# Performance work log

Measured on AMD Instinct MI355X. Metric: run time of the kernel, lower is better.

The kernel has to match this reference:

```python
import jax, jax.numpy as jnp
import numpy as np


def fwht(x):
    """Fast Walsh-Hadamard transform over the last dim (power of 2), normalized by 1/sqrt(n)."""
    n = x.shape[-1]
    orig_shape = x.shape
    x = x.reshape(-1, n)
    h = 1
    while h < n:
        x = x.reshape(-1, n // (2 * h), 2, h)
        a = x[:, :, 0, :]
        b = x[:, :, 1, :]
        x = jnp.stack([a + b, a - b], axis=2)
        h *= 2
    x = x.reshape(orig_shape)
    return x * (1.0 / jnp.sqrt(jnp.asarray(n, dtype=x.dtype)))


def act_quant(x, bits):
    """Per-token absmax symmetric quantization with straight-through estimator."""
    qb = 2.0 ** (bits - 1) - 1.0  # 127 for 8 bits
    scale = qb / jnp.clip(jnp.max(jnp.abs(x), axis=-1, keepdims=True), 1e-5, None)
    q = jnp.clip(jnp.round(x * scale), -qb, qb) / scale
    return x + jax.lax.stop_gradient(q - x)


def weight_quant(w):
    """BitNet b1.58 ternary weight quantization (per-tensor mean-abs scale) with STE."""
    scale = jnp.clip(jnp.mean(jnp.abs(w)), 1e-5, None)
    q = jnp.clip(jnp.round(w / scale), -1.0, 1.0) * scale
    return w + jax.lax.stop_gradient(q - w)


def hbitlinear(x, w, bits):
    # Hadamard rotate activations, quantize acts + ternary weights, then GEMM.
    xh = fwht(x)
    xq = act_quant(xh, bits)
    wq = weight_quant(w)
    return jnp.einsum('bsh,oh->bso', xq, wq)


def setup_inputs() -> dict:
    key = jax.random.key(0)
    k1, k2, k3 = jax.random.split(key, 3)
    B, S, H = 4, 2048, 2048
    I = 4096  # intermediate = hidden * mlp_ratio(2.0)
    hidden_states = jax.random.normal(k1, (B, S, H), dtype=jnp.float32)
    w_up = jax.random.normal(k2, (I, H), dtype=jnp.float32) * 0.02
    w_down = jax.random.normal(k3, (H, I), dtype=jnp.float32) * 0.02
    return {"hidden_states": hidden_states, "w_up": w_up, "w_down": w_down}


def reference(hidden_states, w_up, w_down):
    ACT_BITS = 8
    h = hbitlinear(hidden_states, w_up, ACT_BITS)   # (B, S, I)
    h = jnp.square(jax.nn.relu(h))                  # ReLU^2
    # dropout with p=0.0 (eval/identity)
    out = hbitlinear(h, w_down, ACT_BITS)           # (B, S, H)
    return out
```

## Files before the change

kernel.cpp:

```cpp
#include <hip/hip_runtime.h>
#include <hip/hip_bf16.h>

typedef int i32x4 __attribute__((ext_vector_type(4)));

#define BM 128
#define BN 128
#define BK 64

#define GLL16(g, l) __builtin_amdgcn_global_load_lds( \
    (const __attribute__((address_space(1))) void*)(g), \
    (__attribute__((address_space(3))) void*)(l), 16, 0, 0)

__global__ __launch_bounds__(256) void abs_sum_kernel(const float* __restrict__ w, int n4,
                                                      double* __restrict__ out)
{
    double acc = 0.0;
    const float4* w4 = (const float4*)w;
    for (int i = blockIdx.x * blockDim.x + threadIdx.x; i < n4; i += gridDim.x * blockDim.x) {
        float4 v = w4[i];
        acc += (double)fabsf(v.x) + (double)fabsf(v.y) + (double)fabsf(v.z) + (double)fabsf(v.w);
    }
    for (int o = 32; o > 0; o >>= 1) acc += __shfl_down(acc, o, 64);
    __shared__ double part[4];
    int lane = threadIdx.x & 63, wv = threadIdx.x >> 6;
    if (lane == 0) part[wv] = acc;
    __syncthreads();
    if (threadIdx.x == 0) atomicAdd(out, part[0] + part[1] + part[2] + part[3]);
}

__global__ __launch_bounds__(256) void wquant_kernel(const float* __restrict__ w, int n4,
                                                     const double* __restrict__ sum, double inv_count,
                                                     char* __restrict__ out)
{
    float s = (float)(sum[0] * inv_count);
    s = fmaxf(s, 1e-5f);
    const float4* w4 = (const float4*)w;
    char4* o4 = (char4*)out;
    for (int i = blockIdx.x * blockDim.x + threadIdx.x; i < n4; i += gridDim.x * blockDim.x) {
        float4 v = w4[i];
        char4 c;
        c.x = (char)fminf(fmaxf(rintf(v.x / s), -1.0f), 1.0f);
        c.y = (char)fminf(fmaxf(rintf(v.y / s), -1.0f), 1.0f);
        c.z = (char)fminf(fmaxf(rintf(v.z / s), -1.0f), 1.0f);
        c.w = (char)fminf(fmaxf(rintf(v.w / s), -1.0f), 1.0f);
        o4[i] = c;
    }
}

template<int NS>
__device__ __forceinline__ void hreg(float* v)
{
    #pragma unroll
    for (int h = 1; h < (1 << NS); h <<= 1)
        #pragma unroll
        for (int i = 0; i < 16; i++)
            if ((i & h) == 0) { float a = v[i], b = v[i + h]; v[i] = a + b; v[i + h] = a - b; }
}

template<int N, int TOKS>
__global__ __launch_bounds__(256) void fwht_quant_kernel(
    const float* __restrict__ in, long in_stride,
    char* __restrict__ outq, long out_stride,
    float* __restrict__ scales)
{
    constexpr int L = 256 / TOKS;
    static_assert(N == 16 * L, "N must be 16*threads-per-token");
    __shared__ float sx[TOKS * N];
    __shared__ float red[4];

    const int tid = threadIdx.x;
    const int tk  = tid / L;
    const int lt  = tid % L;
    const long tok = (long)blockIdx.x * TOKS + tk;
    const float* row = in + tok * in_stride;
    float* s = sx + tk * N;

    float v[16];
    {
        const float4* r4 = (const float4*)(row + (size_t)lt * 16);
        float4 a[4];
        #pragma unroll
        for (int i = 0; i < 4; i++) a[i] = r4[i];
        #pragma unroll
        for (int i = 0; i < 4; i++) {
            v[4*i] = a[i].x; v[4*i+1] = a[i].y; v[4*i+2] = a[i].z; v[4*i+3] = a[i].w;
        }
    }
    hreg<4>(v);
    #pragma unroll
    for (int i = 0; i < 4; i++)
        *(float4*)(s + lt * 16 + 4 * i) = make_float4(v[4*i], v[4*i+1], v[4*i+2], v[4*i+3]);
    __syncthreads();

    const int o = lt & 15, ss = lt >> 4;
    #pragma unroll
    for (int j = 0; j < 16; j++) v[j] = s[o + 256 * ss + 16 * j];
    hreg<(L == 256) ? 4 : 3>(v);
    #pragma unroll
    for (int j = 0; j < 16; j++) s[o + 256 * ss + 16 * j] = v[j];
    __syncthreads();

    #pragma unroll
    for (int j = 0; j < 16; j++) v[j] = s[o + 16 * ss + L * j];
    hreg<4>(v);

    const float rn = 1.0f / sqrtf((float)N);
    float m = 0.0f;
    #pragma unroll
    for (int j = 0; j < 16; j++) { v[j] *= rn; m = fmaxf(m, fabsf(v[j])); }
    for (int off = 32; off > 0; off >>= 1) m = fmaxf(m, __shfl_down(m, off, 64));
    if ((tid & 63) == 0) red[tid >> 6] = m;
    __syncthreads();
    float mm;
    if (TOKS == 1) mm = fmaxf(fmaxf(red[0], red[1]), fmaxf(red[2], red[3]));
    else           mm = fmaxf(red[2 * tk], red[2 * tk + 1]);
    mm = fmaxf(mm, 1e-5f);
    const float sc = 127.0f / mm;
    if (lt == 0) scales[tok] = sc;
    __syncthreads();

    char* ct = (char*)sx + tk * N;
    #pragma unroll
    for (int j = 0; j < 16; j++) {
        float q = fminf(fmaxf(rintf(v[j] * sc), -127.0f), 127.0f);
        ct[o + 16 * ss + L * j] = (char)q;
    }
    __syncthreads();
    int4* dst = (int4*)(outq + tok * out_stride);
    dst[lt] = ((const int4*)ct)[lt];
}

__global__ __launch_bounds__(256) void gemm_bt_kernel(
    const char* __restrict__ A, int lda,
    const char* __restrict__ B, int ldb,
    float* __restrict__ C, int ldc,
    int K, int lognx,
    const float* __restrict__ sx,
    const double* __restrict__ wsum, double inv_count,
    int do_relu2)
{
    __shared__ __align__(16) char As[2][BM * BK];
    __shared__ __align__(16) char Bs[2][BN * BK];

    const int bid = blockIdx.x;
    const int xcd = bid & 7;
    const int n = bid >> 3;
    const int nper = gridDim.x >> 3;
    const int bx = n & ((1 << lognx) - 1);
    const int by = xcd * (nper >> lognx) + (n >> lognx);
    const int row0 = by * BM;
    const int col0 = bx * BN;

    const int tid = threadIdx.x;
    const int lane = tid & 63;
    const int wave = tid >> 6;
    const int wm = (wave >> 1) * 64;
    const int wn = (wave & 1) * 64;

    i32x4 acc[4][4] = {};

    const int srow = wave * 16 + (lane >> 2);
    const int scol = (lane & 3) * 16;
    const char* Ag = A + (size_t)(row0 + srow) * lda + scol;
    const char* Bg = B + (size_t)(col0 + srow) * ldb + scol;
    const size_t ldA64 = (size_t)64 * lda, ldB64 = (size_t)64 * ldb;
    const int wb0 = (wave * 16) * BK;
    const int wb1 = (wave * 16 + 64) * BK;

    const int fr = lane & 15;
    const int fk = (lane >> 4) * 16;

    for (int k0 = 0; k0 < K; k0 += 2 * BK) {
        __syncthreads();
        GLL16(Ag + k0,              &As[0][wb0]);
        GLL16(Ag + k0 + ldA64,      &As[0][wb1]);
        GLL16(Bg + k0,              &Bs[0][wb0]);
        GLL16(Bg + k0 + ldB64,      &Bs[0][wb1]);
        GLL16(Ag + k0 + BK,         &As[1][wb0]);
        GLL16(Ag + k0 + BK + ldA64, &As[1][wb1]);
        GLL16(Bg + k0 + BK,         &Bs[1][wb0]);
        GLL16(Bg + k0 + BK + ldB64, &Bs[1][wb1]);
        __syncthreads();

        #pragma unroll
        for (int p = 0; p < 2; p++) {
            i32x4 af[4], bfr[4];
            #pragma unroll
            for (int i = 0; i < 4; i++) {
                af[i]  = *(const i32x4*)(&As[p][(wm + i * 16 + fr) * BK + fk]);
                bfr[i] = *(const i32x4*)(&Bs[p][(wn + i * 16 + fr) * BK + fk]);
            }
            #pragma unroll
            for (int i = 0; i < 4; i++)
                #pragma unroll
                for (int j = 0; j < 4; j++)
                    acc[i][j] = __builtin_amdgcn_mfma_i32_16x16x64_i8(af[i], bfr[j], acc[i][j], 0, 0, 0);
        }
    }

    float sw = (float)(wsum[0] * inv_count);
    sw = fmaxf(sw, 1e-5f);
    const int qd = lane >> 4;
    #pragma unroll
    for (int i = 0; i < 4; i++) {
        #pragma unroll
        for (int r = 0; r < 4; r++) {
            int rowm = row0 + wm + i * 16 + qd * 4 + r;
            float esc = sw / sx[rowm];
            float* crow = C + (size_t)rowm * ldc + col0 + wn;
            #pragma unroll
            for (int j = 0; j < 4; j++) {
                float v = (float)acc[i][j][r] * esc;
                if (do_relu2) { v = fmaxf(v, 0.0f); v = v * v; }
                crow[j * 16 + fr] = v;
            }
        }
    }
}

extern "C" void kernel_launch(void* const* d_in, const int* in_sizes, int n_in,
                              void* d_out, int out_size, void* d_ws, size_t ws_size,
                              hipStream_t stream)
{
    const float* X   = (const float*)d_in[0];
    const float* Wup = (const float*)d_in[1];
    const float* Wdn = (const float*)d_in[2];
    float* out = (float*)d_out;

    const int Mtok = 8192, H = 2048, I = 4096;
    const int NW = H * I;

    char* ws = (char*)d_ws;
    double* sums = (double*)ws;
    float* sx1 = (float*)(ws + 1024);
    float* sx2 = (float*)(ws + 1024 + 32768);
    char* wqup = ws + (1 << 20);
    char* wqdn = wqup + (size_t)NW;
    char* xq1  = wqdn + (size_t)NW;
    float* hbuf = (float*)(xq1 + (size_t)Mtok * H);

    hipMemsetAsync(sums, 0, 16, stream);
    abs_sum_kernel<<<512, 256, 0, stream>>>(Wup, NW / 4, &sums[0]);
    abs_sum_kernel<<<512, 256, 0, stream>>>(Wdn, NW / 4, &sums[1]);
    const double invc = 1.0 / (double)NW;
    wquant_kernel<<<1024, 256, 0, stream>>>(Wup, NW / 4, &sums[0], invc, wqup);
    wquant_kernel<<<1024, 256, 0, stream>>>(Wdn, NW / 4, &sums[1], invc, wqdn);

    fwht_quant_kernel<2048, 2><<<Mtok / 2, 256, 0, stream>>>(X, H, xq1, H, sx1);
    gemm_bt_kernel<<<(I / BN) * (Mtok / BM), 256, 0, stream>>>(
        xq1, H, wqup, H, hbuf, I, H, 5, sx1, &sums[0], invc, 1);
    fwht_quant_kernel<4096, 1><<<Mtok, 256, 0, stream>>>(hbuf, I, (char*)hbuf, 4 * I, sx2);
    gemm_bt_kernel<<<(H / BN) * (Mtok / BM), 256, 0, stream>>>(
        (const char*)hbuf, 4 * I, wqdn, I, out, H, I, 4, sx2, &sums[1], invc, 0);
}
```

Before: 406.2 us.

## Enlarge int8 GEMM tiles to 256x256 with 4-stage LDS pipeline and swizzle

Reworks the int8 MFMA GEMM to 256x256 block tiles over 8 waves. Global-to-LDS loads now run through a 4-buffer ring that keeps three stages in flight, synchronised with explicit vmcnt waits and barriers. An XOR swizzle on LDS addresses is meant to avoid bank conflicts, and setprio raises priority around the MFMA bursts. The goal is more data reuse per block and better overlap of loads with compute. The cost is 128KB of LDS per block and fewer blocks in the grid, so occupancy and the tail effect become risks.

After: 405.8 us. Within noise of the previous version (-0.1%).

```diff
diff --git a/kernel.cpp b/kernel.cpp
--- a/kernel.cpp
+++ b/kernel.cpp
@@ -2,14 +2,12 @@
 #include <hip/hip_bf16.h>
 
 typedef int i32x4 __attribute__((ext_vector_type(4)));
-
-#define BM 128
-#define BN 128
-#define BK 64
 
 #define GLL16(g, l) __builtin_amdgcn_global_load_lds( \
     (const __attribute__((address_space(1))) void*)(g), \
     (__attribute__((address_space(3))) void*)(l), 16, 0, 0)
+
+#define CFENCE() asm volatile("" ::: "memory")
 
 __global__ __launch_bounds__(256) void abs_sum_kernel(const float* __restrict__ w, int n4,
                                                       double* __restrict__ out)
@@ -130,7 +128,11 @@
     dst[lt] = ((const int4*)ct)[lt];
 }
 
-__global__ __launch_bounds__(256) void gemm_bt_kernel(
+#define BM2 256
+#define BN2 256
+#define BK2 64
+
+__global__ __launch_bounds__(512, 2) void gemm_bt_kernel(
     const char* __restrict__ A, int lda,
     const char* __restrict__ B, int ldb,
     float* __restrict__ C, int ldc,
@@ -139,8 +141,8 @@
     const double* __restrict__ wsum, double inv_count,
     int do_relu2)
 {
-    __shared__ __align__(16) char As[2][BM * BK];
-    __shared__ __align__(16) char Bs[2][BN * BK];
+    __shared__ __align__(16) char As[4][BM2 * BK2];
+    __shared__ __align__(16) char Bs[4][BN2 * BK2];
 
     const int bid = blockIdx.x;
     const int xcd = bid & 7;
@@ -148,68 +150,95 @@
     const int nper = gridDim.x >> 3;
     const int bx = n & ((1 << lognx) - 1);
     const int by = xcd * (nper >> lognx) + (n >> lognx);
-    const int row0 = by * BM;
-    const int col0 = bx * BN;
+    const int row0 = by * BM2;
+    const int col0 = bx * BN2;
 
     const int tid = threadIdx.x;
     const int lane = tid & 63;
-    const int wave = tid >> 6;
-    const int wm = (wave >> 1) * 64;
-    const int wn = (wave & 1) * 64;
-
-    i32x4 acc[4][4] = {};
-
-    const int srow = wave * 16 + (lane >> 2);
-    const int scol = (lane & 3) * 16;
-    const char* Ag = A + (size_t)(row0 + srow) * lda + scol;
-    const char* Bg = B + (size_t)(col0 + srow) * ldb + scol;
-    const size_t ldA64 = (size_t)64 * lda, ldB64 = (size_t)64 * ldb;
-    const int wb0 = (wave * 16) * BK;
-    const int wb1 = (wave * 16 + 64) * BK;
+    const int w = tid >> 6;
+    const int wr = w >> 2;
+    const int wc = w & 3;
+
+    i32x4 acc[8][4] = {};
+
+    const int srow = w * 16 + (lane >> 2);
+    const int sseg = ((lane & 3) ^ ((lane >> 3) & 3)) << 4;
+    const char* Ag0 = A + (size_t)(row0 + srow) * lda + sseg;
+    const char* Ag1 = Ag0 + (size_t)128 * lda;
+    const char* Bg0 = B + (size_t)(col0 + srow) * ldb + sseg;
+    const char* Bg1 = Bg0 + (size_t)128 * ldb;
+    const int wdst = w * 1024;
 
     const int fr = lane & 15;
-    const int fk = (lane >> 4) * 16;
-
-    for (int k0 = 0; k0 < K; k0 += 2 * BK) {
-        __syncthreads();
-        GLL16(Ag + k0,              &As[0][wb0]);
-        GLL16(Ag + k0 + ldA64,      &As[0][wb1]);
-        GLL16(Bg + k0,              &Bs[0][wb0]);
-        GLL16(Bg + k0 + ldB64,      &Bs[0][wb1]);
-        GLL16(Ag + k0 + BK,         &As[1][wb0]);
-        GLL16(Ag + k0 + BK + ldA64, &As[1][wb1]);
-        GLL16(Bg + k0 + BK,         &Bs[1][wb0]);
-        GLL16(Bg + k0 + BK + ldB64, &Bs[1][wb1]);
-        __syncthreads();
-
-        #pragma unroll
-        for (int p = 0; p < 2; p++) {
-            i32x4 af[4], bfr[4];
+    const int fks = lane >> 4;
+    const int rsw = ((fks ^ ((fr >> 1) & 3)) << 4);
+    const int aoff = (wr * 128 + fr) * BK2 + rsw;
+    const int boff = (wc * 64  + fr) * BK2 + rsw;
+
+    const int NT = K >> 6;
+
+    auto stage = [&](int tt) {
+        const int sb = tt & 3;
+        const int ko = tt * BK2;
+        GLL16(Ag0 + ko, &As[sb][wdst]);
+        GLL16(Ag1 + ko, &As[sb][wdst + 8192]);
+        GLL16(Bg0 + ko, &Bs[sb][wdst]);
+        GLL16(Bg1 + ko, &Bs[sb][wdst + 8192]);
+    };
+    auto compute = [&](int cb) {
+        const char* as = As[cb];
+        const char* bs = Bs[cb];
+        i32x4 af[8], bf[4];
+        #pragma unroll
+        for (int i = 0; i < 8; ++i) af[i] = *(const i32x4*)(as + aoff + i * 1024);
+        #pragma unroll
+        for (int j = 0; j < 4; ++j) bf[j] = *(const i32x4*)(bs + boff + j * 1024);
+        __builtin_amdgcn_s_setprio(1);
+        #pragma unroll
+        for (int i = 0; i < 8; ++i)
             #pragma unroll
-            for (int i = 0; i < 4; i++) {
-                af[i]  = *(const i32x4*)(&As[p][(wm + i * 16 + fr) * BK + fk]);
-                bfr[i] = *(const i32x4*)(&Bs[p][(wn + i * 16 + fr) * BK + fk]);
-            }
-            #pragma unroll
-            for (int i = 0; i < 4; i++)
-                #pragma unroll
-                for (int j = 0; j < 4; j++)
-                    acc[i][j] = __builtin_amdgcn_mfma_i32_16x16x64_i8(af[i], bfr[j], acc[i][j], 0, 0, 0);
-        }
-    }
+            for (int j = 0; j < 4; ++j)
+                acc[i][j] = __builtin_amdgcn_mfma_i32_16x16x64_i8(af[i], bf[j], acc[i][j], 0, 0, 0);
+        __builtin_amdgcn_s_setprio(0);
+    };
+
+    stage(0); stage(1); stage(2);
+    asm volatile("s_waitcnt vmcnt(8)" ::: "memory");
+    __builtin_amdgcn_s_barrier();
+    CFENCE();
+
+    int t = 0;
+    for (; t < NT - 3; ++t) {
+        stage(t + 3);
+        compute(t & 3);
+        asm volatile("s_waitcnt vmcnt(8)" ::: "memory");
+        __builtin_amdgcn_s_barrier();
+        CFENCE();
+    }
+    compute(t & 3);
+    asm volatile("s_waitcnt vmcnt(4)" ::: "memory");
+    __builtin_amdgcn_s_barrier();
+    CFENCE();
+    ++t;
+    compute(t & 3);
+    asm volatile("s_waitcnt vmcnt(0)" ::: "memory");
+    __builtin_amdgcn_s_barrier();
+    CFENCE();
+    ++t;
+    compute(t & 3);
 
     float sw = (float)(wsum[0] * inv_count);
     sw = fmaxf(sw, 1e-5f);
     const int qd = lane >> 4;
     #pragma unroll
-    for (int i = 0; i < 4; i++) {
-        #pragma unroll
-        for (int r = 0; r < 4; r++) {
-            int rowm = row0 + wm + i * 16 + qd * 4 + r;
+    for (int i = 0; i < 8; ++i) {
+        #pragma unroll
+        for (int r = 0; r < 4; ++r) {
+            int rowm = row0 + wr * 128 + i * 16 + qd * 4 + r;
             float esc = sw / sx[rowm];
-            float* crow = C + (size_t)rowm * ldc + col0 + wn;
+            float* crow = C + (size_t)rowm * ldc + col0 + wc * 64;
             #pragma unroll
-            for (int j = 0; j < 4; j++) {
+            for (int j = 0; j < 4; ++j) {
                 float v = (float)acc[i][j][r] * esc;
                 if (do_relu2) { v = fmaxf(v, 0.0f); v = v * v; }
                 crow[j * 16 + fr] = v;
@@ -247,9 +276,9 @@
     wquant_kernel<<<1024, 256, 0, stream>>>(Wdn, NW / 4, &sums[1], invc, wqdn);
 
     fwht_quant_kernel<2048, 2><<<Mtok / 2, 256, 0, stream>>>(X, H, xq1, H, sx1);
-    gemm_bt_kernel<<<(I / BN) * (Mtok / BM), 256, 0, stream>>>(
-        xq1, H, wqup, H, hbuf, I, H, 5, sx1, &sums[0], invc, 1);
+    gemm_bt_kernel<<<(I / BN2) * (Mtok / BM2), 512, 0, stream>>>(
+        xq1, H, wqup, H, hbuf, I, H, 4, sx1, &sums[0], invc, 1);
     fwht_quant_kernel<4096, 1><<<Mtok, 256, 0, stream>>>(hbuf, I, (char*)hbuf, 4 * I, sx2);
-    gemm_bt_kernel<<<(H / BN) * (Mtok / BM), 256, 0, stream>>>(
-        (const char*)hbuf, 4 * I, wqdn, I, out, H, I, 4, sx2, &sums[1], invc, 0);
-}
+    gemm_bt_kernel<<<(H / BN2) * (Mtok / BM2), 512, 0, stream>>>(
+        (const char*)hbuf, 4 * I, wqdn, I, out, H, I, 3, sx2, &sums[1], invc, 0);
+}
```
